# Kernel tuning notes

Hardware: AMD Instinct MI355X
Metric: run time of the kernel (lower is better)

Reference implementation:

```python
import jax, jax.numpy as jnp
import numpy as np

N_NODES = 50000
N_EDGES = 800000
IN_DIM, HID_DIM, LAT_DIM = 512, 512, 128


def _glorot(key, shape):
    fan_in = shape[0]
    return jax.random.normal(key, shape, dtype=jnp.float32) / np.sqrt(fan_in)


def setup_inputs() -> dict:
    key = jax.random.key(0)
    ks = jax.random.split(key, 10)
    x = jax.random.normal(ks[0], (N_NODES, IN_DIM), dtype=jnp.float32)
    edge_index = jax.random.randint(ks[1], (2, N_EDGES), 0, N_NODES, dtype=jnp.int64)
    edge_weight = jax.random.uniform(ks[2], (N_EDGES,), dtype=jnp.float32)
    return {
        "x": x,
        "edge_index": edge_index,
        "edge_weight": edge_weight,
        "W1": _glorot(ks[3], (IN_DIM, HID_DIM)), "b1": jnp.zeros((HID_DIM,), jnp.float32),
        "W2": _glorot(ks[4], (HID_DIM, LAT_DIM)), "b2": jnp.zeros((LAT_DIM,), jnp.float32),
        "W3": _glorot(ks[5], (LAT_DIM, HID_DIM)), "b3": jnp.zeros((HID_DIM,), jnp.float32),
        "W4": _glorot(ks[6], (HID_DIM, IN_DIM)), "b4": jnp.zeros((IN_DIM,), jnp.float32),
    }


def gcn_conv(x, W, b, src, dst, ew, n_nodes):
    """PyG GCNConv: out = D^{-1/2}(A+I)D^{-1/2} X W + b, self-loop weight 1."""
    xw = x @ W  # [N, out_dim]
    # degree over edges + self-loops (self-loop weight = 1)
    deg = jax.ops.segment_sum(ew, dst, num_segments=n_nodes) + 1.0  # [N]
    dinv = jnp.where(deg > 0, jax.lax.rsqrt(deg), 0.0)
    norm = dinv[src] * ew * dinv[dst]  # [E]
    msg = norm[:, None] * xw[src]      # [E, out_dim] per-edge gather
    agg = jax.ops.segment_sum(msg, dst, num_segments=n_nodes)  # scatter-add
    agg = agg + (dinv * dinv)[:, None] * xw  # self-loop contribution
    return agg + b


def reference(x, edge_index, edge_weight, W1, b1, W2, b2, W3, b3, W4, b4):
    src, dst = edge_index[0], edge_index[1]
    n = x.shape[0]
    # encode
    h = jax.nn.relu(gcn_conv(x, W1, b1, src, dst, edge_weight, n))
    z = gcn_conv(h, W2, b2, src, dst, edge_weight, n)
    # decode (dropout is identity in eval mode)
    h2 = jax.nn.relu(gcn_conv(z, W3, b3, src, dst, edge_weight, n))
    x_recon = gcn_conv(h2, W4, b4, src, dst, edge_weight, n)
    return (x_recon, z)
```

## Files before the change

### kernel.cpp

```cpp
#include <hip/hip_runtime.h>


typedef short bf16x8 __attribute__((ext_vector_type(8)));
typedef float f32x4 __attribute__((ext_vector_type(4)));
typedef float f32x2 __attribute__((ext_vector_type(2)));

__device__ __forceinline__ float bf2f(unsigned short u) {
  return __uint_as_float(((unsigned int)u) << 16);
}
__device__ __forceinline__ unsigned short f2bf(float f) {
  unsigned int u = __float_as_uint(f);
  return (unsigned short)((u + 0x7fffu + ((u >> 16) & 1u)) >> 16);
}

__device__ __forceinline__ void gload_lds16(const void* g, void* l) {
  __builtin_amdgcn_global_load_lds(
      (const __attribute__((address_space(1))) unsigned int*)g,
      (__attribute__((address_space(3))) unsigned int*)l, 16, 0, 0);
}


__global__ void deg_hist_kernel(const int* __restrict__ dst, const float* __restrict__ ew,
                                float* __restrict__ deg, int* __restrict__ cnt, int E) {
  int e = blockIdx.x * blockDim.x + threadIdx.x;
  if (e >= E) return;
  int d = dst[e];
  atomicAdd(&deg[d], ew[e]);
  atomicAdd(&cnt[d], 1);
}

__global__ void block_sums_dinv_kernel(const int* __restrict__ cnt,
                                       const float* __restrict__ deg,
                                       int* __restrict__ sums,
                                       float* __restrict__ dinv, int n) {
  __shared__ int sh[512];
  int i = blockIdx.x * 512 + threadIdx.x;
  int v = 0;
  if (i < n) {
    v = cnt[i];
    dinv[i] = rsqrtf(deg[i] + 1.0f);
  }
  sh[threadIdx.x] = v;
  __syncthreads();
  for (int s = 256; s > 0; s >>= 1) {
    if (threadIdx.x < s) sh[threadIdx.x] += sh[threadIdx.x + s];
    __syncthreads();
  }
  if (threadIdx.x == 0) sums[blockIdx.x] = sh[0];
}

__global__ void scan_sums_kernel(int* sums, int nb) {
  __shared__ int sh[512];
  int t = threadIdx.x;
  int v = (t < nb) ? sums[t] : 0;
  sh[t] = v;
  __syncthreads();
  for (int off = 1; off < 512; off <<= 1) {
    int y = (t >= off) ? sh[t - off] : 0;
    __syncthreads();
    sh[t] += y;
    __syncthreads();
  }
  if (t < nb) sums[t] = sh[t] - v;
}

__global__ void scan_final_kernel(const int* __restrict__ cnt, const int* __restrict__ sums,
                                  int* __restrict__ rowPtr, int* __restrict__ fill, int n) {
  __shared__ int sh[512];
  int i = blockIdx.x * 512 + threadIdx.x;
  int v = (i < n) ? cnt[i] : 0;
  sh[threadIdx.x] = v;
  __syncthreads();
  for (int off = 1; off < 512; off <<= 1) {
    int y = (threadIdx.x >= off) ? sh[threadIdx.x - off] : 0;
    __syncthreads();
    sh[threadIdx.x] += y;
    __syncthreads();
  }
  if (i < n) {
    int incl = sh[threadIdx.x];
    int base = sums[blockIdx.x];
    int excl = base + incl - v;
    rowPtr[i] = excl;
    fill[i] = excl;
    if (i == n - 1) rowPtr[n] = base + incl;
  }
}

__global__ void scatter_edges_kernel(const int* __restrict__ src, const int* __restrict__ dst,
                                     const float* __restrict__ ew, const float* __restrict__ dinv,
                                     int* __restrict__ fill, int2* __restrict__ pk, int E) {
  int e = blockIdx.x * blockDim.x + threadIdx.x;
  if (e >= E) return;
  int s = src[e], d = dst[e];
  int p = atomicAdd(&fill[d], 1);
  float v = dinv[s] * ew[e] * dinv[d];
  pk[p] = make_int2(s, __float_as_int(v));
}


__device__ __forceinline__ void tile_one(const float* __restrict__ W,
                                         short* __restrict__ hi,
                                         int K, int N, int g) {
  int kb_cnt = K >> 6;
  int c = g & 1023;
  int t = g >> 10;
  int kb = t % kb_cnt;
  int nb = t / kb_cnt;
  int colg = (nb << 7) + (c >> 3);
  int k0 = (kb << 6) + (((c & 7) ^ ((c >> 3) & 7)) << 3);
  bf16x8 h8;
#pragma unroll
  for (int j = 0; j < 8; ++j) {
    float w = W[(size_t)(k0 + j) * N + colg];
    h8[j] = (short)f2bf(w);
  }
  *(bf16x8*)(hi + (size_t)g * 8) = h8;
}

__global__ void tile_w4_kernel(const float* __restrict__ W1, short* __restrict__ h1,
                               const float* __restrict__ W2, short* __restrict__ h2,
                               const float* __restrict__ W3, short* __restrict__ h3,
                               const float* __restrict__ W4, short* __restrict__ h4) {
  int g = blockIdx.x * 256 + threadIdx.x;
  if (g < 32768) tile_one(W1, h1, 512, 512, g);
  else if (g < 40960) tile_one(W2, h2, 512, 128, g - 32768);
  else if (g < 49152) tile_one(W3, h3, 128, 512, g - 40960);
  else tile_one(W4, h4, 512, 512, g - 49152);
}


template <int BN, int NC, bool AF32, bool BIAS, bool RELU>
__global__ __launch_bounds__(2 * BN) void mfma_gemm(
    const void* __restrict__ Aptr, const short* __restrict__ Bhi,
    const float* __restrict__ bias, unsigned short* __restrict__ C,
    int M, int N, int K) {
  constexpr int W = BN / 32;
  constexpr int RW = 128 / W;
  constexpr int IA = RW / 8;
  constexpr int NH = BN / 128;
  constexpr int WH = W / NH;
  constexpr int CW = BN / 64;

  __shared__ short As[8192];
  __shared__ short Bs[BN * 64];

  const int nwg = gridDim.x;
  const int orig = blockIdx.x;
  const int xcd = orig & 7;
  const int idx = orig >> 3;
  const int q = nwg >> 3, r = nwg & 7;
  const int wgid = (xcd < r ? xcd * (q + 1) : r * (q + 1) + (xcd - r) * q) + idx;
  const int rowb = wgid / NC;
  const int colb = wgid - rowb * NC;

  const int tid = threadIdx.x;
  const int lane = tid & 63;
  const int wave = tid >> 6;
  const int rowblk = rowb << 7;
  const int colblk = colb * BN;
  const int wr = (wave / CW) << 6;
  const int wc = (wave % CW) << 6;
  const int lr = lane & 15;
  const int lk = lane >> 4;
  const int kbN = K >> 6;
  const int half = wave / WH;
  const int wh = wave % WH;
  const int nb0 = colblk >> 7;

  f32x4 acc[4][4];
#pragma unroll
  for (int i = 0; i < 4; ++i)
#pragma unroll
    for (int j = 0; j < 4; ++j) {
      f32x4 z = {0.f, 0.f, 0.f, 0.f};
      acc[i][j] = z;
    }

  size_t aoff[IA];
#pragma unroll
  for (int i = 0; i < IA; ++i) {
    int rg = rowblk + wave * RW + i * 8 + (lane >> 3);
    if (AF32) rg = (rg < M) ? rg : (M - 1);
    aoff[i] = (size_t)rg * K + (size_t)(((lane & 7) ^ ((lane >> 3) & 7)) << 3);
  }
  short* AsW = As + wave * (RW * 64);
  short* BsW = Bs + half * 8192 + wh * 2048;

  for (int kb = 0; kb < kbN; ++kb) {
    const short* bsrc = Bhi + ((size_t)(nb0 + half) * kbN + kb) * 8192 + (size_t)(wh * 256 + lane) * 8;
#pragma unroll
    for (int i = 0; i < 4; ++i)
      gload_lds16(bsrc + i * 512, BsW + i * 512);
#pragma unroll
    for (int i = 0; i < IA; ++i) {
      if (AF32) {
        const float* ap = (const float*)Aptr + aoff[i] + (kb << 6);
        float4 f0 = *(const float4*)ap;
        float4 f1 = *(const float4*)(ap + 4);
        bf16x8 t;
        t[0] = (short)f2bf(f0.x); t[1] = (short)f2bf(f0.y);
        t[2] = (short)f2bf(f0.z); t[3] = (short)f2bf(f0.w);
        t[4] = (short)f2bf(f1.x); t[5] = (short)f2bf(f1.y);
        t[6] = (short)f2bf(f1.z); t[7] = (short)f2bf(f1.w);
        *(bf16x8*)(AsW + i * 512 + lane * 8) = t;
      } else {
        gload_lds16((const unsigned short*)Aptr + aoff[i] + (kb << 6), AsW + i * 512);
      }
    }
    __syncthreads();
#pragma unroll
    for (int kk = 0; kk < 2; ++kk) {
      bf16x8 af[4], bhf[4];
      const int kc = kk * 4 + lk;
#pragma unroll
      for (int rb = 0; rb < 4; ++rb) {
        int rowl = wr + rb * 16 + lr;
        af[rb] = *(const bf16x8*)(As + rowl * 64 + ((kc ^ (rowl & 7)) << 3));
      }
#pragma unroll
      for (int cb = 0; cb < 4; ++cb) {
        int coll = wc + cb * 16 + lr;
        bhf[cb] = *(const bf16x8*)(Bs + coll * 64 + ((kc ^ (coll & 7)) << 3));
      }
#pragma unroll
      for (int rb = 0; rb < 4; ++rb)
#pragma unroll
        for (int cb = 0; cb < 4; ++cb)
          acc[rb][cb] = __builtin_amdgcn_mfma_f32_16x16x32_bf16(af[rb], bhf[cb], acc[rb][cb], 0, 0, 0);
    }
    __syncthreads();
  }

#pragma unroll
  for (int cb = 0; cb < 4; ++cb) {
    int colg = colblk + wc + cb * 16 + lr;
    float badd = BIAS ? bias[colg] : 0.0f;
#pragma unroll
    for (int rb = 0; rb < 4; ++rb) {
#pragma unroll
      for (int i = 0; i < 4; ++i) {
        int row = rowblk + wr + rb * 16 + lk * 4 + i;
        float v = acc[rb][cb][i] + badd;
        if (RELU) v = fmaxf(v, 0.f);
        C[(size_t)row * N + colg] = f2bf(v);
      }
    }
  }
}


template <int PT, bool INF32>
__device__ __forceinline__ void load_row(const void* p, size_t off, float* xv) {
  if (INF32) {
    if (PT == 2) {
      f32x2 f = *(const f32x2*)((const float*)p + off);
      xv[0] = f[0]; xv[1] = f[1];
    } else {
      f32x4 f0 = *(const f32x4*)((const float*)p + off);
      f32x4 f1 = *(const f32x4*)((const float*)p + off + 4);
      xv[0] = f0[0]; xv[1] = f0[1]; xv[2] = f0[2]; xv[3] = f0[3];
      xv[4] = f1[0]; xv[5] = f1[1]; xv[6] = f1[2]; xv[7] = f1[3];
    }
  } else {
    if (PT == 2) {
      unsigned int u = *(const unsigned int*)((const unsigned short*)p + off);
      xv[0] = bf2f((unsigned short)(u & 0xffffu));
      xv[1] = bf2f((unsigned short)(u >> 16));
    } else {
      bf16x8 r = *(const bf16x8*)((const short*)p + off);
#pragma unroll
      for (int j = 0; j < 8; ++j) xv[j] = bf2f((unsigned short)r[j]);
    }
  }
}

template <int PT, int UF, bool INF32, bool BIAS, bool RELU, bool W32, bool W16>
__global__ __launch_bounds__(256) void agg_kernel(
    const void* __restrict__ xw, const int2* __restrict__ pk,
    const int* __restrict__ rowPtr, const float* __restrict__ dinv,
    const float* __restrict__ bias, float* __restrict__ out32,
    unsigned short* __restrict__ out16, int n) {
  const int DIM = PT * 64;
  int node = blockIdx.x * 4 + (threadIdx.x >> 6);
  if (node >= n) return;
  int t = threadIdx.x & 63;
  float acc[PT];
#pragma unroll
  for (int q = 0; q < PT; ++q) acc[q] = 0.f;

  int beg = rowPtr[node], end = rowPtr[node + 1];
  int e = beg;
  for (; e + UF <= end; e += UF) {
    int2 p[UF];
    float xv[UF][PT];
#pragma unroll
    for (int u = 0; u < UF; ++u) p[u] = pk[e + u];
#pragma unroll
    for (int u = 0; u < UF; ++u)
      load_row<PT, INF32>(xw, (size_t)p[u].x * DIM + t * PT, xv[u]);
#pragma unroll
    for (int u = 0; u < UF; ++u) {
      float v = __int_as_float(p[u].y);
#pragma unroll
      for (int q = 0; q < PT; ++q) acc[q] += v * xv[u][q];
    }
  }
  for (; e < end; ++e) {
    int2 pe = pk[e];
    float v = __int_as_float(pe.y);
    float xv[PT];
    load_row<PT, INF32>(xw, (size_t)pe.x * DIM + t * PT, xv);
#pragma unroll
    for (int q = 0; q < PT; ++q) acc[q] += v * xv[q];
  }
  float di = dinv[node];
  float sl = di * di;
  {
    float xv[PT];
    load_row<PT, INF32>(xw, (size_t)node * DIM + t * PT, xv);
#pragma unroll
    for (int q = 0; q < PT; ++q) acc[q] += sl * xv[q];
  }
  if (BIAS) {
#pragma unroll
    for (int q = 0; q < PT; ++q) acc[q] += bias[t * PT + q];
  }
  if (RELU) {
#pragma unroll
    for (int q = 0; q < PT; ++q) acc[q] = fmaxf(acc[q], 0.f);
  }
  if (W32) {
    if (PT == 2) {
      f32x2 o;
      o[0] = acc[0]; o[1] = acc[1];
      *(f32x2*)(out32 + (size_t)node * DIM + t * PT) = o;
    } else {
      f32x4 o0, o1;
      o0[0] = acc[0]; o0[1] = acc[1]; o0[2] = acc[2]; o0[3] = acc[3];
      o1[0] = acc[4 % PT]; o1[1] = acc[5 % PT]; o1[2] = acc[6 % PT]; o1[3] = acc[7 % PT];
      *(f32x4*)(out32 + (size_t)node * DIM + t * PT) = o0;
      *(f32x4*)(out32 + (size_t)node * DIM + t * PT + 4) = o1;
    }
  }
  if (W16) {
    if (PT == 2) {
      unsigned int u = (unsigned int)f2bf(acc[0]) | ((unsigned int)f2bf(acc[1]) << 16);
      *(unsigned int*)(out16 + (size_t)node * DIM + t * PT) = u;
    } else {
      bf16x8 o;
#pragma unroll
      for (int j = 0; j < PT; ++j) o[j % 8] = (short)f2bf(acc[j]);
      *(bf16x8*)(out16 + (size_t)node * DIM + t * PT) = o;
    }
  }
}


extern "C" void kernel_launch(void* const* d_in, const int* in_sizes, int n_in,
                              void* d_out, int out_size, void* d_ws, size_t ws_size,
                              hipStream_t stream) {
  const float* x  = (const float*)d_in[0];
  const int*   ei = (const int*)d_in[1];
  const float* ew = (const float*)d_in[2];
  const float* W1 = (const float*)d_in[3];
  const float* b1 = (const float*)d_in[4];
  const float* W2 = (const float*)d_in[5];
  const float* b2 = (const float*)d_in[6];
  const float* W3 = (const float*)d_in[7];
  const float* b3 = (const float*)d_in[8];
  const float* W4 = (const float*)d_in[9];
  const float* b4 = (const float*)d_in[10];

  const int n = in_sizes[0] / 512;
  const int E = in_sizes[2];
  const int MB128 = (n + 127) / 128;
  const int Mpad = MB128 * 128;

  float* out   = (float*)d_out;
  float* z_out = out + (size_t)n * 512;

  char* w = (char*)d_ws;
  auto alloc = [&](size_t bytes) {
    char* p = w;
    w += (bytes + 255) & ~(size_t)255;
    return p;
  };
  float* deg    = (float*)alloc((size_t)n * 4);
  float* dinv   = (float*)alloc((size_t)n * 4);
  int*   cnt    = (int*)alloc((size_t)n * 4);
  int*   rowPtr = (int*)alloc((size_t)(n + 1) * 4);
  int*   fill   = (int*)alloc((size_t)n * 4);
  int*   sums   = (int*)alloc(4096);
  int2*  pk     = (int2*)alloc((size_t)E * 8);
  short* whi1 = (short*)alloc((size_t)512 * 512 * 2);
  short* whi2 = (short*)alloc((size_t)512 * 128 * 2);
  short* whi3 = (short*)alloc((size_t)128 * 512 * 2);
  short* whi4 = (short*)alloc((size_t)512 * 512 * 2);
  unsigned short* T  = (unsigned short*)alloc((size_t)Mpad * 128 * 2);
  unsigned short* B1 = (unsigned short*)alloc((size_t)Mpad * 512 * 2);
  unsigned short* B2 = (unsigned short*)alloc((size_t)Mpad * 512 * 2);

  unsigned short* zbf = B2;

  const int* srcp = ei;
  const int* dstp = ei + E;

  hipMemsetAsync(deg, 0, (size_t)n * 4, stream);
  hipMemsetAsync(cnt, 0, (size_t)n * 4, stream);
  deg_hist_kernel<<<(E + 255) / 256, 256, 0, stream>>>(dstp, ew, deg, cnt, E);
  int NB = (n + 511) / 512;
  block_sums_dinv_kernel<<<NB, 512, 0, stream>>>(cnt, deg, sums, dinv, n);
  scan_sums_kernel<<<1, 512, 0, stream>>>(sums, NB);
  scan_final_kernel<<<NB, 512, 0, stream>>>(cnt, sums, rowPtr, fill, n);
  scatter_edges_kernel<<<(E + 255) / 256, 256, 0, stream>>>(srcp, dstp, ew, dinv, fill, pk, E);

  tile_w4_kernel<<<320, 256, 0, stream>>>(W1, whi1, W2, whi2, W3, whi3, W4, whi4);

  const int AGB = (n + 3) / 4;

  mfma_gemm<256, 2, true, false, false><<<2 * MB128, 512, 0, stream>>>(
      x, whi1, nullptr, B2, n, 512, 512);
  agg_kernel<8, 4, false, true, true, false, true><<<AGB, 256, 0, stream>>>(
      B2, pk, rowPtr, dinv, b1, nullptr, B1, n);

  mfma_gemm<128, 1, false, false, false><<<MB128, 256, 0, stream>>>(
      B1, whi2, nullptr, T, Mpad, 128, 512);
  agg_kernel<2, 8, false, true, false, true, true><<<AGB, 256, 0, stream>>>(
      T, pk, rowPtr, dinv, b2, z_out, zbf, n);

  agg_kernel<2, 8, false, false, false, false, true><<<AGB, 256, 0, stream>>>(
      zbf, pk, rowPtr, dinv, nullptr, nullptr, T, n);
  mfma_gemm<256, 2, false, true, true><<<2 * MB128, 512, 0, stream>>>(
      T, whi3, b3, B2, Mpad, 512, 128);

  mfma_gemm<256, 2, false, false, false><<<2 * MB128, 512, 0, stream>>>(
      B2, whi4, nullptr, B1, Mpad, 512, 512);
  agg_kernel<8, 4, false, true, false, true, false><<<AGB, 256, 0, stream>>>(
      B1, pk, rowPtr, dinv, b4, out, nullptr, n);
}
```

Baseline: 599.9 us.

## Double-buffer GEMM LDS tiles with K=32 stages to overlap loads and MFMA

The bf16 MFMA GEMM now keeps two LDS buffers for A and B and uses a K-step of 32 instead of 64. The loads for the next K-block are issued before the MFMAs on the current block, leaving one barrier per iteration instead of two. The weight pre-tiling kernel and the LDS swizzle are rewritten to match the 32-wide K panels. The aim is to hide global-load latency behind compute, at the cost of twice as many loop iterations and a load-to-barrier distance of only one stage. For the fp32 A path the synchronous loads and bf16 conversion now sit in front of the MFMAs.

```diff
diff --git a/kernel.cpp b/kernel.cpp
--- a/kernel.cpp
+++ b/kernel.cpp
@@ -102,13 +102,15 @@
 __device__ __forceinline__ void tile_one(const float* __restrict__ W,
                                          short* __restrict__ hi,
                                          int K, int N, int g) {
-  int kb_cnt = K >> 6;
-  int c = g & 1023;
-  int t = g >> 10;
+  int kb_cnt = K >> 5;
+  int c = g & 511;
+  int t = g >> 9;
   int kb = t % kb_cnt;
   int nb = t / kb_cnt;
-  int colg = (nb << 7) + (c >> 3);
-  int k0 = (kb << 6) + (((c & 7) ^ ((c >> 3) & 7)) << 3);
+  int col_in = c >> 2;
+  int slot = c & 3;
+  int colg = (nb << 7) + col_in;
+  int k0 = (kb << 5) + ((slot ^ (col_in & 3)) << 3);
   bf16x8 h8;
 #pragma unroll
   for (int j = 0; j < 8; ++j) {
@@ -136,14 +138,13 @@
     const float* __restrict__ bias, unsigned short* __restrict__ C,
     int M, int N, int K) {
   constexpr int W = BN / 32;
-  constexpr int RW = 128 / W;
-  constexpr int IA = RW / 8;
+  constexpr int IA = 512 / (64 * W);
   constexpr int NH = BN / 128;
-  constexpr int WH = W / NH;
+  constexpr int IB = (512 * NH) / (64 * W);
   constexpr int CW = BN / 64;
 
-  __shared__ short As[8192];
-  __shared__ short Bs[BN * 64];
+  __shared__ unsigned short As[2][4096];
+  __shared__ unsigned short Bs[2][NH * 4096];
 
   const int nwg = gridDim.x;
   const int orig = blockIdx.x;
@@ -163,9 +164,7 @@
   const int wc = (wave % CW) << 6;
   const int lr = lane & 15;
   const int lk = lane >> 4;
-  const int kbN = K >> 6;
-  const int half = wave / WH;
-  const int wh = wave % WH;
+  const int kbN = K >> 5;
   const int nb0 = colblk >> 7;
 
   f32x4 acc[4][4];
@@ -177,25 +176,23 @@
       acc[i][j] = z;
     }
 
-  size_t aoff[IA];
+  int arow[IA], akoff[IA], admp[IA];
 #pragma unroll
   for (int i = 0; i < IA; ++i) {
-    int rg = rowblk + wave * RW + i * 8 + (lane >> 3);
+    int c = i * 64 * W + wave * 64 + lane;
+    int row = c >> 2, slot = c & 3;
+    int rg = rowblk + row;
     if (AF32) rg = (rg < M) ? rg : (M - 1);
-    aoff[i] = (size_t)rg * K + (size_t)(((lane & 7) ^ ((lane >> 3) & 7)) << 3);
-  }
-  short* AsW = As + wave * (RW * 64);
-  short* BsW = Bs + half * 8192 + wh * 2048;
-
-  for (int kb = 0; kb < kbN; ++kb) {
-    const short* bsrc = Bhi + ((size_t)(nb0 + half) * kbN + kb) * 8192 + (size_t)(wh * 256 + lane) * 8;
-#pragma unroll
-    for (int i = 0; i < 4; ++i)
-      gload_lds16(bsrc + i * 512, BsW + i * 512);
+    arow[i] = rg;
+    akoff[i] = (slot ^ (row & 3)) << 3;
+    admp[i] = c * 8;
+  }
+
+  auto stageA = [&](int buf, int kb) {
 #pragma unroll
     for (int i = 0; i < IA; ++i) {
       if (AF32) {
-        const float* ap = (const float*)Aptr + aoff[i] + (kb << 6);
+        const float* ap = (const float*)Aptr + (size_t)arow[i] * K + (kb << 5) + akoff[i];
         float4 f0 = *(const float4*)ap;
         float4 f1 = *(const float4*)(ap + 4);
         bf16x8 t;
@@ -203,33 +200,55 @@
         t[2] = (short)f2bf(f0.z); t[3] = (short)f2bf(f0.w);
         t[4] = (short)f2bf(f1.x); t[5] = (short)f2bf(f1.y);
         t[6] = (short)f2bf(f1.z); t[7] = (short)f2bf(f1.w);
-        *(bf16x8*)(AsW + i * 512 + lane * 8) = t;
+        *(bf16x8*)&As[buf][admp[i]] = t;
       } else {
-        gload_lds16((const unsigned short*)Aptr + aoff[i] + (kb << 6), AsW + i * 512);
+        const unsigned short* src =
+            (const unsigned short*)Aptr + (size_t)arow[i] * K + (kb << 5) + akoff[i];
+        gload_lds16(src, &As[buf][(size_t)(i * 64 * W + wave * 64) * 8]);
       }
     }
-    __syncthreads();
-#pragma unroll
-    for (int kk = 0; kk < 2; ++kk) {
-      bf16x8 af[4], bhf[4];
-      const int kc = kk * 4 + lk;
-#pragma unroll
-      for (int rb = 0; rb < 4; ++rb) {
-        int rowl = wr + rb * 16 + lr;
-        af[rb] = *(const bf16x8*)(As + rowl * 64 + ((kc ^ (rowl & 7)) << 3));
-      }
-#pragma unroll
-      for (int cb = 0; cb < 4; ++cb) {
-        int coll = wc + cb * 16 + lr;
-        bhf[cb] = *(const bf16x8*)(Bs + coll * 64 + ((kc ^ (coll & 7)) << 3));
-      }
-#pragma unroll
-      for (int rb = 0; rb < 4; ++rb)
-#pragma unroll
-        for (int cb = 0; cb < 4; ++cb)
-          acc[rb][cb] = __builtin_amdgcn_mfma_f32_16x16x32_bf16(af[rb], bhf[cb], acc[rb][cb], 0, 0, 0);
-    }
-    __syncthreads();
+  };
+
+  auto stageB = [&](int buf, int kb) {
+#pragma unroll
+    for (int j = 0; j < IB; ++j) {
+      int cB = j * 64 * W + wave * 64;
+      int panel = cB >> 9;
+      int cin = (cB & 511) + lane;
+      const short* src = Bhi + (((size_t)(nb0 + panel)) * kbN + kb) * 4096 + (size_t)cin * 8;
+      gload_lds16(src, &Bs[buf][(size_t)cB * 8]);
+    }
+  };
+
+  stageA(0, 0);
+  stageB(0, 0);
+  __syncthreads();
+
+  int buf = 0;
+  for (int kb = 0; kb < kbN; ++kb) {
+    if (kb + 1 < kbN) {
+      stageA(buf ^ 1, kb + 1);
+      stageB(buf ^ 1, kb + 1);
+    }
+    bf16x8 af[4], bh[4];
+#pragma unroll
+    for (int rb = 0; rb < 4; ++rb) {
+      int rowl = wr + rb * 16 + lr;
+      af[rb] = *(const bf16x8*)&As[buf][rowl * 32 + ((lk ^ (rowl & 3)) << 3)];
+    }
+#pragma unroll
+    for (int cb = 0; cb < 4; ++cb) {
+      int coll = wc + cb * 16 + lr;
+      bh[cb] = *(const bf16x8*)&Bs[buf][(coll >> 7) * 4096 + (coll & 127) * 32 +
+                                        ((lk ^ (coll & 3)) << 3)];
+    }
+#pragma unroll
+    for (int rb = 0; rb < 4; ++rb)
+#pragma unroll
+      for (int cb = 0; cb < 4; ++cb)
+        acc[rb][cb] = __builtin_amdgcn_mfma_f32_16x16x32_bf16(af[rb], bh[cb], acc[rb][cb], 0, 0, 0);
+    __syncthreads();
+    buf ^= 1;
   }
 
 #pragma unroll
```

New measurement: 616.1 us. +2.7%, slower.
